# Optimization experiments

Measured on AMD Instinct MI355X. Metric: run time of the kernel, lower is better.

Reference implementation:

```python
import jax, jax.numpy as jnp
import numpy as np

ORDER = 3  # truncation level; num_components = ORDER*(ORDER+1)//2 = 6 (independent weights)


def setup_inputs() -> dict:
    key = jax.random.key(0)
    k1, k2, k3 = jax.random.split(key, 3)
    B, T, D, F = 64, 4096, 128, 64
    C = ORDER * (ORDER + 1) // 2
    sequences = jax.random.normal(k1, (B, T, D), dtype=jnp.float32)
    # ls2t_uniform-style init: scaled uniform per component
    kernel = jax.random.normal(k2, (C, D, F), dtype=jnp.float32) / np.sqrt(D)
    bias = jax.random.normal(k3, (C, F), dtype=jnp.float32) * 0.01
    return {"sequences": sequences, "kernel": kernel, "bias": bias}


def _exclusive_cumsum(x, axis):
    # exclusive cumsum = inclusive cumsum minus self (avoids concat/pad allocs)
    return jnp.cumsum(x, axis=axis) - x


def reference(sequences, kernel, bias):
    # sequences: [B, T, D]; kernel: [C, D, F]; bias: [C, F]
    # M[c] = sequences @ kernel[c] + bias[c]  -> [C, B, T, F]
    M = jnp.einsum('btd,cdf->cbtf', sequences, kernel) + bias[:, None, None, :]
    # Level 1: plain sum over time of first component
    Y = [jnp.sum(M[0], axis=1)]  # [B, F]
    k = 1
    for m in range(1, ORDER):
        R = M[k]
        k += 1
        for _ in range(m):
            # iterated-sum recursion: strictly-lower-triangular (exclusive) cumsum over time
            R = M[k] * _exclusive_cumsum(R, axis=1)
            k += 1
        Y.append(jnp.sum(R, axis=1))
    return jnp.stack(Y, axis=-1)  # [B, F, ORDER]
```

## Files before the change

kernel.cpp:

```cpp
#include <hip/hip_runtime.h>
#include <hip/hip_bf16.h>


#define B_ 64
#define T_ 4096
#define D_ 128
#define F_ 64
#define TGROUPS 8
#define TB 512
#define CHT 16
#define NITER (TB / CHT)
#define TPB 512
#define RING 3

typedef __attribute__((ext_vector_type(8))) short short8v;
typedef __attribute__((ext_vector_type(4))) float f32x4;
typedef __attribute__((ext_vector_type(4))) unsigned short ushort4v;

__device__ __forceinline__ unsigned short bfb(float x) {
    __hip_bfloat16 h = __float2bfloat16(x);
    unsigned short u;
    __builtin_memcpy(&u, &h, 2);
    return u;
}

#define BAR() asm volatile("s_waitcnt lgkmcnt(0)\n\ts_barrier" ::: "memory")

__global__ __launch_bounds__(TPB, 2)
void ls2t_kernel(const float* __restrict__ seq,
                 const float* __restrict__ kern,
                 const float* __restrict__ bias,
                 float* __restrict__ ws)
{
    __shared__ unsigned short slds[RING][CHT * D_];

    const int tid  = threadIdx.x;
    const int tg   = blockIdx.x;
    const int b    = blockIdx.y;
    const int lane = tid & 63;
    const int w    = tid >> 6;
    const int cg   = w >> 2;
    const int wv   = w & 3;
    const int fr   = lane & 15;
    const int lg   = lane >> 4;
    const int f    = wv * 16 + fr;

    short8v bfrag[3][4];
    float bc[3];
    #pragma unroll
    for (int cc = 0; cc < 3; ++cc) {
        const int c = cg * 3 + cc;
        bc[cc] = bias[c * F_ + f];
        #pragma unroll
        for (int ks = 0; ks < 4; ++ks) {
            const float* kp = kern + ((size_t)c * D_ + ks * 32 + lg * 8) * F_ + f;
            short8v bf;
            #pragma unroll
            for (int j = 0; j < 8; ++j) bf[j] = (short)bfb(kp[(size_t)j * F_]);
            bfrag[cc][ks] = bf;
        }
    }

    const float* sbase = seq + ((size_t)b * T_ + (size_t)tg * TB) * D_;

    const int srow = tid >> 5;
    const int c4   = tid & 31;
    const int skey = srow & 7;
    const float* g0 = sbase + ((size_t)((srow >> 2) * 128 + (srow & 3))) * D_ + c4 * 4;
    const int woff = srow * D_ + 8 * ((c4 >> 1) ^ skey) + 4 * (c4 & 1);

    float4 vA, vB;

    auto issueA = [&](int i) { vA = *reinterpret_cast<const float4*>(g0 + (size_t)i * 4 * D_); };
    auto issueB = [&](int i) { vB = *reinterpret_cast<const float4*>(g0 + (size_t)i * 4 * D_); };
    auto wldsA = [&](int bufi) {
        ushort4v u;
        u[0] = bfb(vA.x); u[1] = bfb(vA.y); u[2] = bfb(vA.z); u[3] = bfb(vA.w);
        *reinterpret_cast<ushort4v*>(&slds[bufi][woff]) = u;
    };
    auto wldsB = [&](int bufi) {
        ushort4v u;
        u[0] = bfb(vB.x); u[1] = bfb(vB.y); u[2] = bfb(vB.z); u[3] = bfb(vB.w);
        *reinterpret_cast<ushort4v*>(&slds[bufi][woff]) = u;
    };

    float a0 = 0.f, s1 = 0.f, s2 = 0.f, q2 = 0.f;
    float su = 0.f, sv = 0.f, sw = 0.f, qvu = 0.f, qwv = 0.f, qwvu = 0.f;

    auto compute = [&](int bufi) {
        f32x4 acc[3];
        #pragma unroll
        for (int cc = 0; cc < 3; ++cc)
            acc[cc] = (f32x4){bc[cc], bc[cc], bc[cc], bc[cc]};

        #pragma unroll
        for (int ks = 0; ks < 4; ++ks) {
            const int m0i = ks * 4 + lg;
            short8v a = *reinterpret_cast<const short8v*>(
                &slds[bufi][fr * D_ + 8 * (m0i ^ (fr & 7))]);
            #pragma unroll
            for (int cc = 0; cc < 3; ++cc)
                acc[cc] = __builtin_amdgcn_mfma_f32_16x16x32_bf16(
                    a, bfrag[cc][ks], acc[cc], 0, 0, 0);
        }

        if (cg == 0) {
            #pragma unroll
            for (int r = 0; r < 4; ++r) {
                float m0 = acc[0][r], m1 = acc[1][r], m2 = acc[2][r];
                a0 += m0;
                q2  = fmaf(m2, s1, q2);
                s2 += m2;
                s1 += m1;
            }
        } else {
            #pragma unroll
            for (int r = 0; r < 4; ++r) {
                float m3 = acc[0][r], m4 = acc[1][r], m5 = acc[2][r];
                qwvu = fmaf(m5, qvu, qwvu);
                qwv  = fmaf(m5, sv, qwv);
                sw  += m5;
                qvu  = fmaf(m4, su, qvu);
                sv  += m4;
                su  += m3;
            }
        }
    };

    issueA(0);
    issueB(1);
    wldsA(0);

    int b0 = 0, b1 = 1, b2 = 2;
    #pragma unroll 1
    for (int i = 0; i < NITER; i += 2) {
        if (i + 2 < NITER) issueA(i + 2);
        wldsB(b1);
        BAR();
        compute(b0);

        if (i + 3 < NITER) issueB(i + 3);
        if (i + 2 < NITER) wldsA(b2);
        BAR();
        compute(b1);

        int nb0 = b2, nb1 = b0, nb2 = b1;
        b0 = nb0; b1 = nb1; b2 = nb2;
    }

    if (cg == 0) {
        #pragma unroll
        for (int m = 16; m <= 32; m <<= 1) {
            float oa0 = __shfl_xor(a0, m), os1 = __shfl_xor(s1, m);
            float os2 = __shfl_xor(s2, m), oq2 = __shfl_xor(q2, m);
            bool up = (lane & m) != 0;
            float Aa0 = up ? oa0 : a0, As1 = up ? os1 : s1;
            float As2 = up ? os2 : s2, Aq2 = up ? oq2 : q2;
            float Ba0 = up ? a0 : oa0, Bs1 = up ? s1 : os1;
            float Bs2 = up ? s2 : os2, Bq2 = up ? q2 : oq2;
            a0 = Aa0 + Ba0;
            q2 = Aq2 + Bq2 + As1 * Bs2;
            s1 = As1 + Bs1;
            s2 = As2 + Bs2;
        }
        if (lg == 0) {
            float* wp = ws + (((size_t)b * TGROUPS + tg) * F_ + f) * 10;
            wp[0] = a0; wp[1] = s1; wp[2] = s2; wp[3] = q2;
        }
    } else {
        #pragma unroll
        for (int m = 16; m <= 32; m <<= 1) {
            float osu = __shfl_xor(su, m),  osv = __shfl_xor(sv, m);
            float osw = __shfl_xor(sw, m),  oqvu = __shfl_xor(qvu, m);
            float oqwv = __shfl_xor(qwv, m), oqwvu = __shfl_xor(qwvu, m);
            bool up = (lane & m) != 0;
            float Asu = up ? osu : su,   Asv = up ? osv : sv;
            float Asw = up ? osw : sw,   Aqvu = up ? oqvu : qvu;
            float Aqwv = up ? oqwv : qwv, Aqwvu = up ? oqwvu : qwvu;
            float Bsu = up ? su : osu,   Bsv = up ? sv : osv;
            float Bsw = up ? sw : osw,   Bqvu = up ? qvu : oqvu;
            float Bqwv = up ? qwv : oqwv, Bqwvu = up ? qwvu : oqwvu;
            qwvu = Aqwvu + Bqwvu + Aqvu * Bsw + Asu * Bqwv;
            qwv  = Aqwv + Bqwv + Asv * Bsw;
            qvu  = Aqvu + Bqvu + Asu * Bsv;
            su = Asu + Bsu;
            sv = Asv + Bsv;
            sw = Asw + Bsw;
        }
        if (lg == 0) {
            float* wp = ws + (((size_t)b * TGROUPS + tg) * F_ + f) * 10;
            wp[4] = su; wp[5] = sv; wp[6] = sw;
            wp[7] = qvu; wp[8] = qwv; wp[9] = qwvu;
        }
    }
}

struct St { float a0, s1, s2, q2, su, sv, sw, qvu, qwv, qwvu; };

__device__ __forceinline__ St mergeSt(const St& A, const St& B) {
    St r;
    r.a0   = A.a0 + B.a0;
    r.q2   = A.q2 + B.q2 + A.s1 * B.s2;
    r.s1   = A.s1 + B.s1;
    r.s2   = A.s2 + B.s2;
    r.qwvu = A.qwvu + B.qwvu + A.qvu * B.sw + A.su * B.qwv;
    r.qwv  = A.qwv + B.qwv + A.sv * B.sw;
    r.qvu  = A.qvu + B.qvu + A.su * B.sv;
    r.su   = A.su + B.su;
    r.sv   = A.sv + B.sv;
    r.sw   = A.sw + B.sw;
    return r;
}

__global__ __launch_bounds__(64)
void ls2t_fold_kernel(const float* __restrict__ ws, float* __restrict__ out)
{
    const int b = blockIdx.x;
    const int f = threadIdx.x;
    St A = {0, 0, 0, 0, 0, 0, 0, 0, 0, 0};
    #pragma unroll
    for (int g = 0; g < TGROUPS; ++g) {
        const float* rp = ws + (((size_t)b * TGROUPS + g) * F_ + f) * 10;
        St r = {rp[0], rp[1], rp[2], rp[3], rp[4],
                rp[5], rp[6], rp[7], rp[8], rp[9]};
        A = mergeSt(A, r);
    }
    float* op = out + ((size_t)b * F_ + f) * 3;
    op[0] = A.a0;
    op[1] = A.q2;
    op[2] = A.qwvu;
}

extern "C" void kernel_launch(void* const* d_in, const int* in_sizes, int n_in,
                              void* d_out, int out_size, void* d_ws, size_t ws_size,
                              hipStream_t stream) {
    const float* seq  = (const float*)d_in[0];
    const float* kern = (const float*)d_in[1];
    const float* bias = (const float*)d_in[2];
    float* out = (float*)d_out;
    float* ws  = (float*)d_ws;

    dim3 g1(TGROUPS, B_);
    ls2t_kernel<<<g1, TPB, 0, stream>>>(seq, kern, bias, ws);
    ls2t_fold_kernel<<<B_, F_, 0, stream>>>(ws, out);
}
```

Measured before the change: 47.93 us.

## Restructure into per-wave private LDS pipelines computing all six components over shorter spans

Each wave now stages its own 16-row time chunk into a private double-buffered LDS region and computes all six projection components itself. This removes the block-wide barriers and the split of components across two wave groups. The time axis is cut into 128-step spans, which launches many more smaller blocks, and the fold kernel merges the larger number of partial states. In exchange, the four waves of a block each load the same sequence rows, so cache traffic rises roughly fourfold, and the bf16 packing now uses perm instructions with a wider swizzle.

```diff
diff --git a/kernel.cpp b/kernel.cpp
--- a/kernel.cpp
+++ b/kernel.cpp
@@ -6,16 +6,15 @@
 #define T_ 4096
 #define D_ 128
 #define F_ 64
-#define TGROUPS 8
-#define TB 512
+#define NC 6
+#define SPAN 128
+#define NSPAN (T_ / SPAN)
 #define CHT 16
-#define NITER (TB / CHT)
-#define TPB 512
-#define RING 3
+#define NITER (SPAN / CHT)
+#define TPB 256
 
 typedef __attribute__((ext_vector_type(8))) short short8v;
 typedef __attribute__((ext_vector_type(4))) float f32x4;
-typedef __attribute__((ext_vector_type(4))) unsigned short ushort4v;
 
 __device__ __forceinline__ unsigned short bfb(float x) {
     __hip_bfloat16 h = __float2bfloat16(x);
@@ -23,8 +22,6 @@
     __builtin_memcpy(&u, &h, 2);
     return u;
 }
-
-#define BAR() asm volatile("s_waitcnt lgkmcnt(0)\n\ts_barrier" ::: "memory")
 
 __global__ __launch_bounds__(TPB, 2)
 void ls2t_kernel(const float* __restrict__ seq,
@@ -32,166 +29,154 @@
                  const float* __restrict__ bias,
                  float* __restrict__ ws)
 {
-    __shared__ unsigned short slds[RING][CHT * D_];
+    __shared__ unsigned short slds[4][2][CHT * D_];
 
     const int tid  = threadIdx.x;
-    const int tg   = blockIdx.x;
+    const int span = blockIdx.x;
     const int b    = blockIdx.y;
     const int lane = tid & 63;
-    const int w    = tid >> 6;
-    const int cg   = w >> 2;
-    const int wv   = w & 3;
+    const int wv   = tid >> 6;
     const int fr   = lane & 15;
     const int lg   = lane >> 4;
     const int f    = wv * 16 + fr;
 
-    short8v bfrag[3][4];
-    float bc[3];
+    short8v bfrag[NC][4];
+    float bc[NC];
     #pragma unroll
-    for (int cc = 0; cc < 3; ++cc) {
-        const int c = cg * 3 + cc;
-        bc[cc] = bias[c * F_ + f];
+    for (int c = 0; c < NC; ++c) {
+        bc[c] = bias[c * F_ + f];
         #pragma unroll
         for (int ks = 0; ks < 4; ++ks) {
             const float* kp = kern + ((size_t)c * D_ + ks * 32 + lg * 8) * F_ + f;
             short8v bf;
             #pragma unroll
             for (int j = 0; j < 8; ++j) bf[j] = (short)bfb(kp[(size_t)j * F_]);
-            bfrag[cc][ks] = bf;
-        }
-    }
-
-    const float* sbase = seq + ((size_t)b * T_ + (size_t)tg * TB) * D_;
-
-    const int srow = tid >> 5;
-    const int c4   = tid & 31;
-    const int skey = srow & 7;
-    const float* g0 = sbase + ((size_t)((srow >> 2) * 128 + (srow & 3))) * D_ + c4 * 4;
-    const int woff = srow * D_ + 8 * ((c4 >> 1) ^ skey) + 4 * (c4 & 1);
-
-    float4 vA, vB;
-
-    auto issueA = [&](int i) { vA = *reinterpret_cast<const float4*>(g0 + (size_t)i * 4 * D_); };
-    auto issueB = [&](int i) { vB = *reinterpret_cast<const float4*>(g0 + (size_t)i * 4 * D_); };
-    auto wldsA = [&](int bufi) {
-        ushort4v u;
-        u[0] = bfb(vA.x); u[1] = bfb(vA.y); u[2] = bfb(vA.z); u[3] = bfb(vA.w);
-        *reinterpret_cast<ushort4v*>(&slds[bufi][woff]) = u;
+            bfrag[c][ks] = bf;
+        }
+    }
+
+    const float* sbase = seq + ((size_t)b * T_ + (size_t)span * SPAN) * D_;
+
+    const int srow0 = lane >> 5;
+    const int sd4   = lane & 31;
+
+    unsigned short* const L0 = &slds[wv][0][0];
+    unsigned short* const L1 = &slds[wv][1][0];
+
+    float4 fA[8];
+
+    auto issue = [&](int i) {
+        #pragma unroll
+        for (int k = 0; k < 8; ++k) {
+            const int row = 2 * k + srow0;
+            const int tl  = (row >> 2) * 32 + (row & 3) + i * 4;
+            fA[k] = *reinterpret_cast<const float4*>(
+                sbase + (size_t)tl * D_ + sd4 * 4);
+        }
     };
-    auto wldsB = [&](int bufi) {
-        ushort4v u;
-        u[0] = bfb(vB.x); u[1] = bfb(vB.y); u[2] = bfb(vB.z); u[3] = bfb(vB.w);
-        *reinterpret_cast<ushort4v*>(&slds[bufi][woff]) = u;
+
+    auto packw = [&](unsigned short* L) {
+        #pragma unroll
+        for (int k = 0; k < 8; ++k) {
+            const int row = 2 * k + srow0;
+            unsigned u0 = __float_as_uint(fA[k].x);
+            unsigned u1 = __float_as_uint(fA[k].y);
+            unsigned u2 = __float_as_uint(fA[k].z);
+            unsigned u3 = __float_as_uint(fA[k].w);
+            unsigned p0 = __builtin_amdgcn_perm(u1, u0, 0x07060302u);
+            unsigned p1 = __builtin_amdgcn_perm(u3, u2, 0x07060302u);
+            const int off = row * 128 + (((sd4 >> 1) ^ (row & 15)) << 3)
+                          + ((sd4 & 1) << 2);
+            uint2 pv; pv.x = p0; pv.y = p1;
+            *reinterpret_cast<uint2*>(&L[off]) = pv;
+        }
     };
 
     float a0 = 0.f, s1 = 0.f, s2 = 0.f, q2 = 0.f;
     float su = 0.f, sv = 0.f, sw = 0.f, qvu = 0.f, qwv = 0.f, qwvu = 0.f;
 
-    auto compute = [&](int bufi) {
-        f32x4 acc[3];
-        #pragma unroll
-        for (int cc = 0; cc < 3; ++cc)
-            acc[cc] = (f32x4){bc[cc], bc[cc], bc[cc], bc[cc]};
+    auto compute = [&](const unsigned short* L) {
+        f32x4 acc[NC];
+        #pragma unroll
+        for (int c = 0; c < NC; ++c)
+            acc[c] = (f32x4){bc[c], bc[c], bc[c], bc[c]};
 
         #pragma unroll
         for (int ks = 0; ks < 4; ++ks) {
-            const int m0i = ks * 4 + lg;
-            short8v a = *reinterpret_cast<const short8v*>(
-                &slds[bufi][fr * D_ + 8 * (m0i ^ (fr & 7))]);
+            const int unit = (ks * 4 + lg) ^ (fr & 15);
+            short8v a = *reinterpret_cast<const short8v*>(&L[fr * 128 + unit * 8]);
             #pragma unroll
-            for (int cc = 0; cc < 3; ++cc)
-                acc[cc] = __builtin_amdgcn_mfma_f32_16x16x32_bf16(
-                    a, bfrag[cc][ks], acc[cc], 0, 0, 0);
-        }
-
-        if (cg == 0) {
-            #pragma unroll
-            for (int r = 0; r < 4; ++r) {
-                float m0 = acc[0][r], m1 = acc[1][r], m2 = acc[2][r];
-                a0 += m0;
-                q2  = fmaf(m2, s1, q2);
-                s2 += m2;
-                s1 += m1;
-            }
-        } else {
-            #pragma unroll
-            for (int r = 0; r < 4; ++r) {
-                float m3 = acc[0][r], m4 = acc[1][r], m5 = acc[2][r];
-                qwvu = fmaf(m5, qvu, qwvu);
-                qwv  = fmaf(m5, sv, qwv);
-                sw  += m5;
-                qvu  = fmaf(m4, su, qvu);
-                sv  += m4;
-                su  += m3;
-            }
+            for (int c = 0; c < NC; ++c)
+                acc[c] = __builtin_amdgcn_mfma_f32_16x16x32_bf16(
+                    a, bfrag[c][ks], acc[c], 0, 0, 0);
+        }
+
+        #pragma unroll
+        for (int r = 0; r < 4; ++r) {
+            float m0 = acc[0][r], m1 = acc[1][r], m2 = acc[2][r];
+            float m3 = acc[3][r], m4 = acc[4][r], m5 = acc[5][r];
+            a0  += m0;
+            q2   = fmaf(m2, s1, q2);
+            s2  += m2;
+            s1  += m1;
+            qwvu = fmaf(m5, qvu, qwvu);
+            qwv  = fmaf(m5, sv, qwv);
+            sw  += m5;
+            qvu  = fmaf(m4, su, qvu);
+            sv  += m4;
+            su  += m3;
         }
     };
 
-    issueA(0);
-    issueB(1);
-    wldsA(0);
-
-    int b0 = 0, b1 = 1, b2 = 2;
+    issue(0);
+    packw(L0);
+    issue(1);
+
     #pragma unroll 1
     for (int i = 0; i < NITER; i += 2) {
-        if (i + 2 < NITER) issueA(i + 2);
-        wldsB(b1);
-        BAR();
-        compute(b0);
-
-        if (i + 3 < NITER) issueB(i + 3);
-        if (i + 2 < NITER) wldsA(b2);
-        BAR();
-        compute(b1);
-
-        int nb0 = b2, nb1 = b0, nb2 = b1;
-        b0 = nb0; b1 = nb1; b2 = nb2;
-    }
-
-    if (cg == 0) {
-        #pragma unroll
-        for (int m = 16; m <= 32; m <<= 1) {
-            float oa0 = __shfl_xor(a0, m), os1 = __shfl_xor(s1, m);
-            float os2 = __shfl_xor(s2, m), oq2 = __shfl_xor(q2, m);
-            bool up = (lane & m) != 0;
-            float Aa0 = up ? oa0 : a0, As1 = up ? os1 : s1;
-            float As2 = up ? os2 : s2, Aq2 = up ? oq2 : q2;
-            float Ba0 = up ? a0 : oa0, Bs1 = up ? s1 : os1;
-            float Bs2 = up ? s2 : os2, Bq2 = up ? q2 : oq2;
-            a0 = Aa0 + Ba0;
-            q2 = Aq2 + Bq2 + As1 * Bs2;
-            s1 = As1 + Bs1;
-            s2 = As2 + Bs2;
-        }
-        if (lg == 0) {
-            float* wp = ws + (((size_t)b * TGROUPS + tg) * F_ + f) * 10;
-            wp[0] = a0; wp[1] = s1; wp[2] = s2; wp[3] = q2;
-        }
-    } else {
-        #pragma unroll
-        for (int m = 16; m <= 32; m <<= 1) {
-            float osu = __shfl_xor(su, m),  osv = __shfl_xor(sv, m);
-            float osw = __shfl_xor(sw, m),  oqvu = __shfl_xor(qvu, m);
-            float oqwv = __shfl_xor(qwv, m), oqwvu = __shfl_xor(qwvu, m);
-            bool up = (lane & m) != 0;
-            float Asu = up ? osu : su,   Asv = up ? osv : sv;
-            float Asw = up ? osw : sw,   Aqvu = up ? oqvu : qvu;
-            float Aqwv = up ? oqwv : qwv, Aqwvu = up ? oqwvu : qwvu;
-            float Bsu = up ? su : osu,   Bsv = up ? sv : osv;
-            float Bsw = up ? sw : osw,   Bqvu = up ? qvu : oqvu;
-            float Bqwv = up ? qwv : oqwv, Bqwvu = up ? qwvu : oqwvu;
-            qwvu = Aqwvu + Bqwvu + Aqvu * Bsw + Asu * Bqwv;
-            qwv  = Aqwv + Bqwv + Asv * Bsw;
-            qvu  = Aqvu + Bqvu + Asu * Bsv;
-            su = Asu + Bsu;
-            sv = Asv + Bsv;
-            sw = Asw + Bsw;
-        }
-        if (lg == 0) {
-            float* wp = ws + (((size_t)b * TGROUPS + tg) * F_ + f) * 10;
-            wp[4] = su; wp[5] = sv; wp[6] = sw;
-            wp[7] = qvu; wp[8] = qwv; wp[9] = qwvu;
-        }
+        compute(L0);
+        packw(L1);
+        if (i + 2 < NITER) issue(i + 2);
+        compute(L1);
+        if (i + 2 < NITER) packw(L0);
+        if (i + 3 < NITER) issue(i + 3);
+    }
+
+    #pragma unroll
+    for (int m = 16; m <= 32; m <<= 1) {
+        float oa0 = __shfl_xor(a0, m),   os1 = __shfl_xor(s1, m);
+        float os2 = __shfl_xor(s2, m),   oq2 = __shfl_xor(q2, m);
+        float osu = __shfl_xor(su, m),   osv = __shfl_xor(sv, m);
+        float osw = __shfl_xor(sw, m),   oqvu = __shfl_xor(qvu, m);
+        float oqwv = __shfl_xor(qwv, m), oqwvu = __shfl_xor(qwvu, m);
+        const bool up = (lane & m) != 0;
+        float Aa0 = up ? oa0 : a0,   Ba0 = up ? a0 : oa0;
+        float As1 = up ? os1 : s1,   Bs1 = up ? s1 : os1;
+        float As2 = up ? os2 : s2,   Bs2 = up ? s2 : os2;
+        float Aq2 = up ? oq2 : q2,   Bq2 = up ? q2 : oq2;
+        float Asu = up ? osu : su,   Bsu = up ? su : osu;
+        float Asv = up ? osv : sv,   Bsv = up ? sv : osv;
+        float Asw = up ? osw : sw,   Bsw = up ? sw : osw;
+        float Aqvu = up ? oqvu : qvu,   Bqvu = up ? qvu : oqvu;
+        float Aqwv = up ? oqwv : qwv,   Bqwv = up ? qwv : oqwv;
+        float Aqwvu = up ? oqwvu : qwvu, Bqwvu = up ? qwvu : oqwvu;
+        a0   = Aa0 + Ba0;
+        q2   = Aq2 + Bq2 + As1 * Bs2;
+        s1   = As1 + Bs1;
+        s2   = As2 + Bs2;
+        qwvu = Aqwvu + Bqwvu + Aqvu * Bsw + Asu * Bqwv;
+        qwv  = Aqwv + Bqwv + Asv * Bsw;
+        qvu  = Aqvu + Bqvu + Asu * Bsv;
+        su   = Asu + Bsu;
+        sv   = Asv + Bsv;
+        sw   = Asw + Bsw;
+    }
+
+    if (lg == 0) {
+        float* wp = ws + (((size_t)b * NSPAN + span) * F_ + f) * 10;
+        wp[0] = a0;  wp[1] = s1;  wp[2] = s2;  wp[3] = q2;
+        wp[4] = su;  wp[5] = sv;  wp[6] = sw;
+        wp[7] = qvu; wp[8] = qwv; wp[9] = qwvu;
     }
 }
 
@@ -219,8 +204,8 @@
     const int f = threadIdx.x;
     St A = {0, 0, 0, 0, 0, 0, 0, 0, 0, 0};
     #pragma unroll
-    for (int g = 0; g < TGROUPS; ++g) {
-        const float* rp = ws + (((size_t)b * TGROUPS + g) * F_ + f) * 10;
+    for (int g = 0; g < NSPAN; ++g) {
+        const float* rp = ws + (((size_t)b * NSPAN + g) * F_ + f) * 10;
         St r = {rp[0], rp[1], rp[2], rp[3], rp[4],
                 rp[5], rp[6], rp[7], rp[8], rp[9]};
         A = mergeSt(A, r);
@@ -240,7 +225,7 @@
     float* out = (float*)d_out;
     float* ws  = (float*)d_ws;
 
-    dim3 g1(TGROUPS, B_);
+    dim3 g1(NSPAN, B_);
     ls2t_kernel<<<g1, TPB, 0, stream>>>(seq, kern, bias, ws);
     ls2t_fold_kernel<<<B_, F_, 0, stream>>>(ws, out);
 }
```

Result: slower. 56.20 us (+17.3%).
